# Optimization experiments

Hardware: AMD Instinct MI355X
Metric: run time of the kernel (lower is better)

## Reference

```python
import jax, jax.numpy as jnp
import numpy as np

L = 2          # num_bigbird_encoder_blocks
H = 8          # n_heads
BS = 64        # block_size
G = 2          # num_global_blocks
W = 3          # window_size (blocks)
EPS = 1e-8


def rmsnorm(x, w, eps=EPS):
    return x * jax.lax.rsqrt(jnp.mean(x * x, axis=-1, keepdims=True) + eps) * w


def setup_inputs() -> dict:
    key = jax.random.key(0)
    ks = jax.random.split(key, 12)
    B, S, D, F, V = 8, 2048, 256, 1024, 32000
    nB = S // BS
    inp = {
        "input_ids": jax.random.randint(ks[0], (B, S), 0, V, dtype=jnp.int64),
        "rand_idx": jax.random.randint(ks[1], (nB, 2), 0, nB, dtype=jnp.int32),
        "emb": jax.random.normal(ks[2], (V, D), jnp.float32) * 0.02,
        "ln1_w": jnp.ones((L, D), jnp.float32),
        "wq": jax.random.normal(ks[3], (L, D, D), jnp.float32) / np.sqrt(D),
        "wk": jax.random.normal(ks[4], (L, D, D), jnp.float32) / np.sqrt(D),
        "wv": jax.random.normal(ks[5], (L, D, D), jnp.float32) / np.sqrt(D),
        "wo": jax.random.normal(ks[6], (L, D, D), jnp.float32) / np.sqrt(D),
        "ln2_w": jnp.ones((L, D), jnp.float32),
        "w1": jax.random.normal(ks[7], (L, D, F), jnp.float32) / np.sqrt(D),
        "w2": jax.random.normal(ks[8], (L, F, D), jnp.float32) / np.sqrt(F),
        "final_ln_w": jnp.ones((D,), jnp.float32),
    }
    return inp


def _split_heads(x, B, nB, dh):
    # [B,S,D] -> [B,H,nB,bs,dh]
    return x.reshape(B, nB, BS, H, dh).transpose(0, 3, 1, 2, 4)


def reference(input_ids, rand_idx, emb, ln1_w, wq, wk, wv, wo, ln2_w, w1, w2, final_ln_w):
    B, S = input_ids.shape
    D = emb.shape[1]
    dh = D // H
    nB = S // BS
    scale = 1.0 / np.sqrt(dh)

    # block-sparse key-block indices per query block: global + sliding window + random
    blocks = jnp.arange(nB)
    win = jnp.clip(blocks[:, None] + jnp.arange(-(W // 2), W // 2 + 1)[None, :], 0, nB - 1)
    glob = jnp.broadcast_to(jnp.arange(G), (nB, G))
    idx = jnp.concatenate([glob, win, rand_idx.astype(jnp.int32)], axis=1)  # [nB, M], M=7
    M = idx.shape[1]

    x = emb[input_ids]  # [B,S,D]
    for l in range(L):
        h = rmsnorm(x, ln1_w[l])
        q = _split_heads(h @ wq[l], B, nB, dh)  # [B,H,nB,bs,dh]
        k = _split_heads(h @ wk[l], B, nB, dh)
        v = _split_heads(h @ wv[l], B, nB, dh)
        k_sel = k[:, :, idx]  # [B,H,nB,M,bs,dh]
        v_sel = v[:, :, idx]
        scores = jnp.einsum("bhnqd,bhnmsd->bhnqms", q, k_sel) * scale
        a = jax.nn.softmax(scores.reshape(B, H, nB, BS, M * BS), axis=-1)
        a = a.reshape(B, H, nB, BS, M, BS)
        o = jnp.einsum("bhnqms,bhnmsd->bhnqd", a, v_sel)
        o = o.transpose(0, 2, 3, 1, 4).reshape(B, S, D)
        x = x + o @ wo[l]
        h2 = rmsnorm(x, ln2_w[l])
        x = x + jax.nn.gelu(h2 @ w1[l]) @ w2[l]
    return rmsnorm(x, final_ln_w)
```

## Files before the change

kernel.cpp:

```cpp
#include <hip/hip_runtime.h>
#include <cstdint>
#include <cstddef>

typedef __bf16 bf16x8 __attribute__((ext_vector_type(8)));
typedef __bf16 bf16x4 __attribute__((ext_vector_type(4)));
typedef float  f32x4  __attribute__((ext_vector_type(4)));
typedef unsigned u32x2 __attribute__((ext_vector_type(2)));
typedef unsigned u32x4 __attribute__((ext_vector_type(4)));

#define DMODEL 256

__device__ __forceinline__ float bflo(unsigned u) { return __builtin_bit_cast(float, u << 16); }
__device__ __forceinline__ float bfhi(unsigned u) { return __builtin_bit_cast(float, u & 0xffff0000u); }
__device__ __forceinline__ unsigned short bfbits(float f) {
  return __builtin_bit_cast(unsigned short, (__bf16)f);
}

#define GLOAD_LDS16(gp, lp) __builtin_amdgcn_global_load_lds(                 \
    (const __attribute__((address_space(1))) unsigned*)(gp),                  \
    (__attribute__((address_space(3))) unsigned*)(lp), 16, 0, 0)

__global__ void transpose_all(const float* __restrict__ wq, const float* __restrict__ wk,
                              const float* __restrict__ wv, const float* __restrict__ wo,
                              const float* __restrict__ w1, const float* __restrict__ w2,
                              __bf16* __restrict__ wbase) {
  int idx = blockIdx.x * 256 + threadIdx.x;
  int l = idx >= 786432;
  int r = idx - l * 786432;
  __bf16* wb = wbase + (size_t)l * 786432;
  const float* s; __bf16* d; int R, C, e;
  if (r < 65536)       { s = wq + l * 65536;  d = wb;          R = 256;  C = 256;  e = r; }
  else if (r < 131072) { s = wk + l * 65536;  d = wb + 65536;  R = 256;  C = 256;  e = r - 65536; }
  else if (r < 196608) { s = wv + l * 65536;  d = wb + 131072; R = 256;  C = 256;  e = r - 131072; }
  else if (r < 262144) { s = wo + l * 65536;  d = wb + 196608; R = 256;  C = 256;  e = r - 196608; }
  else if (r < 524288) { s = w1 + l * 262144; d = wb + 262144; R = 256;  C = 1024; e = r - 262144; }
  else                 { s = w2 + l * 262144; d = wb + 524288; R = 1024; C = 256;  e = r - 524288; }
  int row = e / C, col = e - row * C;
  d[col * R + row] = (__bf16)s[e];
}

__global__ void embed_k(const int* __restrict__ ids, const float* __restrict__ emb, float* __restrict__ x) {
  int row = blockIdx.x * 4 + (threadIdx.x >> 6);
  int lane = threadIdx.x & 63;
  int id = ids[row];
  ((f32x4*)(x + (size_t)row * DMODEL))[lane] = ((const f32x4*)(emb + (size_t)id * DMODEL))[lane];
}

template<typename OUT>
__global__ void rmsnorm_k(const float* __restrict__ x, const float* __restrict__ w, OUT* __restrict__ out) {
  int row = blockIdx.x * 4 + (threadIdx.x >> 6);
  int lane = threadIdx.x & 63;
  f32x4 v = ((const f32x4*)(x + (size_t)row * DMODEL))[lane];
  float ss = v[0]*v[0] + v[1]*v[1] + v[2]*v[2] + v[3]*v[3];
  #pragma unroll
  for (int off = 1; off < 64; off <<= 1) ss += __shfl_xor(ss, off);
  float rms = rsqrtf(ss * (1.0f / DMODEL) + 1e-8f);
  f32x4 wv = ((const f32x4*)w)[lane];
  if constexpr (sizeof(OUT) == 4) {
    f32x4 o;
    o[0] = v[0]*rms*wv[0]; o[1] = v[1]*rms*wv[1]; o[2] = v[2]*rms*wv[2]; o[3] = v[3]*rms*wv[3];
    ((f32x4*)((float*)out + (size_t)row * DMODEL))[lane] = o;
  } else {
    bf16x4 o;
    o[0] = (__bf16)(v[0]*rms*wv[0]); o[1] = (__bf16)(v[1]*rms*wv[1]);
    o[2] = (__bf16)(v[2]*rms*wv[2]); o[3] = (__bf16)(v[3]*rms*wv[3]);
    ((bf16x4*)((__bf16*)out + (size_t)row * DMODEL))[lane] = o;
  }
}

__device__ __forceinline__ float gelu_f(float v) {
  return 0.5f * v * (1.0f + tanhf(0.7978845608028654f * (v + 0.044715f * v * v * v)));
}

template<bool RES, bool GELU, bool OUTB>
__launch_bounds__(256)
__global__ void gemm_bt(const __bf16* __restrict__ A, const __bf16* __restrict__ Bt,
                        __bf16* __restrict__ outb, float* __restrict__ res,
                        int K, int N) {
  __shared__ char sm[32768];
  int tid = threadIdx.x;
  int lane = tid & 63;
  int w = tid >> 6;
  int wr = w >> 1, wc = w & 1;
  int lr = lane & 15;
  int hk = lane >> 4;
  size_t bm = (size_t)blockIdx.x * 128, bn = (size_t)blockIdx.y * 128;
  const __bf16* Ab = A + bm * (size_t)K;
  const __bf16* Bb = Bt + bn * (size_t)K;

  int u0 = w * 128 + lane;
  int r0 = u0 >> 2, c0 = u0 & 3;
  int u1 = u0 + 64;
  int r1 = u1 >> 2, c1 = u1 & 3;
  size_t ga0 = (size_t)r0 * K + c0 * 8;
  size_t ga1 = (size_t)r1 * K + c1 * 8;
  int lb0 = (w * 2) * 1024;
  int lb1 = (w * 2 + 1) * 1024;

  int nt = K >> 5;
  GLOAD_LDS16(Ab + ga0, sm + lb0);
  GLOAD_LDS16(Bb + ga0, sm + 8192 + lb0);
  GLOAD_LDS16(Ab + ga1, sm + lb1);
  GLOAD_LDS16(Bb + ga1, sm + 8192 + lb1);
  __syncthreads();

  f32x4 acc[4][4] = {};
  for (int t = 0; t < nt; ++t) {
    char* cur = sm + (t & 1) * 16384;
    if (t + 1 < nt) {
      char* nxt = sm + ((t + 1) & 1) * 16384;
      int kk = (t + 1) * 32;
      GLOAD_LDS16(Ab + ga0 + kk, nxt + lb0);
      GLOAD_LDS16(Bb + ga0 + kk, nxt + 8192 + lb0);
      GLOAD_LDS16(Ab + ga1 + kk, nxt + lb1);
      GLOAD_LDS16(Bb + ga1 + kk, nxt + 8192 + lb1);
    }
    bf16x8 av[4], bv[4];
    #pragma unroll
    for (int i = 0; i < 4; ++i)
      av[i] = *(const bf16x8*)(cur + (wr * 64 + i * 16 + lr) * 64 + hk * 16);
    #pragma unroll
    for (int i = 0; i < 4; ++i)
      bv[i] = *(const bf16x8*)(cur + 8192 + (wc * 64 + i * 16 + lr) * 64 + hk * 16);
    #pragma unroll
    for (int mi = 0; mi < 4; ++mi)
      #pragma unroll
      for (int ni = 0; ni < 4; ++ni)
        acc[mi][ni] = __builtin_amdgcn_mfma_f32_16x16x32_bf16(av[mi], bv[ni], acc[mi][ni], 0, 0, 0);
    __syncthreads();
  }

  size_t row0 = bm + wr * 64 + (hk << 2);
  size_t col0 = bn + wc * 64 + lr;
  #pragma unroll
  for (int mi = 0; mi < 4; ++mi)
    #pragma unroll
    for (int ni = 0; ni < 4; ++ni)
      #pragma unroll
      for (int j = 0; j < 4; ++j) {
        size_t row = row0 + mi * 16 + j, col = col0 + ni * 16;
        float val = acc[mi][ni][j];
        if constexpr (GELU) val = gelu_f(val);
        if constexpr (RES)  res[row * N + col] += val;
        if constexpr (OUTB) outb[row * N + col] = (__bf16)val;
      }
}

#define ATTN_LDS 57344

__launch_bounds__(256)
__global__ void attn_k(const __bf16* __restrict__ qkv, const int* __restrict__ rand_idx,
                       __bf16* __restrict__ o) {
  extern __shared__ char sm[];
  char* smVt = sm + 28672;
  int tid = threadIdx.x;
  int lane = tid & 63;
  int w = tid >> 6;
  int q16 = lane & 15, g = lane >> 4;

  int bid0 = blockIdx.x;
  int bid = (bid0 & 7) * 256 + (bid0 >> 3);
  int b = bid >> 8;
  int hh = (bid >> 5) & 7;
  int n = bid & 31;
  int r5 = rand_idx[n * 2], r6 = rand_idx[n * 2 + 1];
  int nm1 = n > 0 ? n - 1 : 0;
  int np1 = n < 31 ? n + 1 : 31;
  size_t base = (size_t)b * 2048;

  #pragma unroll
  for (int it = 0; it < 7; ++it) {
    int chunk = it * 256 + tid;
    int r = chunk >> 2, c16 = chunk & 3;
    int m = r >> 6, si = r & 63;
    int kb = m == 0 ? 0 : m == 1 ? 1 : m == 2 ? nm1 : m == 3 ? n : m == 4 ? np1 : m == 5 ? r5 : r6;
    u32x4 d = *(const u32x4*)(qkv + (base + kb * 64 + si) * 768 + 256 + hh * 32 + c16 * 8);
    *(u32x4*)(sm + ((chunk * 16) ^ ((r & 7) << 4))) = d;
  }

  #pragma unroll
  for (int it = 0; it < 4; ++it) {
    int item = it * 256 + tid;
    if (item < 896) {
      int dp = item & 15, ko = item >> 4;
      int s0 = ko * 8;
      int m = s0 >> 6, si = s0 & 63;
      int kb = m == 0 ? 0 : m == 1 ? 1 : m == 2 ? nm1 : m == 3 ? n : m == 4 ? np1 : m == 5 ? r5 : r6;
      const unsigned* vs = (const unsigned*)(qkv + (base + kb * 64 + si) * 768 + 512 + hh * 32) + dp;
      unsigned vr[8];
      #pragma unroll
      for (int i = 0; i < 8; ++i) vr[i] = vs[(size_t)i * 384];
      u32x4 lo4, hi4;
      #pragma unroll
      for (int wd = 0; wd < 4; ++wd) {
        unsigned a = vr[2 * wd], bb = vr[2 * wd + 1];
        lo4[wd] = (a & 0xffffu) | (bb << 16);
        hi4[wd] = (a >> 16) | (bb & 0xffff0000u);
      }
      unsigned swz = (unsigned)((dp & 7) << 4);
      int byte0 = (2 * dp) * 896 + ko * 16;
      *(u32x4*)(smVt + (byte0 ^ swz)) = lo4;
      *(u32x4*)(smVt + ((byte0 + 896) ^ swz)) = hi4;
    }
  }

  bf16x8 qf = *(const bf16x8*)(qkv + (base + n * 64 + w * 16 + q16) * 768 + hh * 32 + g * 8);

  __syncthreads();

  const float SC  = 0.17677669529663687f * 1.4426950408889634f;
  const float THR = 8.0f / SC;
  int src0 = q16 + 32 * (g & 1);
  int src1 = src0 + 16;
  bool hi = (g >= 2);
  float m_run = -1e30f, mc = 0.f, ssum = 0.f;
  f32x4 oacc[2] = {};
  bool first = true;

  #pragma unroll
  for (int c = 0; c < 7; ++c) {
    f32x4 st[4];
    #pragma unroll
    for (int tl = 0; tl < 4; ++tl) {
      int row = 16 * (4 * c + tl) + q16;
      bf16x8 kf = *(const bf16x8*)(sm + ((row * 64 + g * 16) ^ ((q16 & 7) << 4)));
      st[tl] = __builtin_amdgcn_mfma_f32_16x16x32_bf16(kf, qf, (f32x4){0.f, 0.f, 0.f, 0.f}, 0, 0, 0);
    }
    float lm = st[0][0];
    #pragma unroll
    for (int tl = 0; tl < 4; ++tl) {
      lm = fmaxf(lm, fmaxf(fmaxf(st[tl][0], st[tl][1]), fmaxf(st[tl][2], st[tl][3])));
    }
    lm = fmaxf(lm, __shfl_xor(lm, 16));
    lm = fmaxf(lm, __shfl_xor(lm, 32));
    if (first || !__all(lm <= m_run + THR)) {
      float nm = fmaxf(m_run, lm);
      float sf = __builtin_amdgcn_exp2f((m_run - nm) * SC);
      ssum *= sf;
      #pragma unroll
      for (int dt = 0; dt < 2; ++dt)
        #pragma unroll
        for (int j = 0; j < 4; ++j) oacc[dt][j] *= sf;
      m_run = nm;
      mc = nm * SC;
      first = false;
    }
    unsigned pk0[4], pk1[4];
    #pragma unroll
    for (int tl = 0; tl < 4; ++tl) {
      float e0 = __builtin_amdgcn_exp2f(fmaf(st[tl][0], SC, -mc));
      float e1 = __builtin_amdgcn_exp2f(fmaf(st[tl][1], SC, -mc));
      float e2 = __builtin_amdgcn_exp2f(fmaf(st[tl][2], SC, -mc));
      float e3 = __builtin_amdgcn_exp2f(fmaf(st[tl][3], SC, -mc));
      ssum += (e0 + e1) + (e2 + e3);
      pk0[tl] = (unsigned)bfbits(e0) | ((unsigned)bfbits(e1) << 16);
      pk1[tl] = (unsigned)bfbits(e2) | ((unsigned)bfbits(e3) << 16);
    }
    #pragma unroll
    for (int ksl = 0; ksl < 2; ++ksl) {
      int ks = 2 * c + ksl;
      int lt0 = 2 * ksl, lt1 = 2 * ksl + 1;
      unsigned a0 = __shfl(pk0[lt0], src0), b0 = __shfl(pk0[lt1], src0);
      unsigned a1 = __shfl(pk1[lt0], src0), b1 = __shfl(pk1[lt1], src0);
      unsigned a2 = __shfl(pk0[lt0], src1), b2 = __shfl(pk0[lt1], src1);
      unsigned a3 = __shfl(pk1[lt0], src1), b3 = __shfl(pk1[lt1], src1);
      u32x4 pw;
      pw[0] = hi ? b0 : a0; pw[1] = hi ? b1 : a1;
      pw[2] = hi ? b2 : a2; pw[3] = hi ? b3 : a3;
      bf16x8 pf = __builtin_bit_cast(bf16x8, pw);
      #pragma unroll
      for (int dt = 0; dt < 2; ++dt) {
        int d = 16 * dt + q16;
        bf16x8 vf = *(const bf16x8*)(smVt + ((d * 896 + 64 * ks + 16 * g) ^ (((d >> 1) & 7) << 4)));
        oacc[dt] = __builtin_amdgcn_mfma_f32_16x16x32_bf16(vf, pf, oacc[dt], 0, 0, 0);
      }
    }
  }

  ssum += __shfl_xor(ssum, 16);
  ssum += __shfl_xor(ssum, 32);
  float inv = 1.0f / ssum;
  size_t orow = (base + n * 64 + w * 16 + q16) * 256 + hh * 32;
  #pragma unroll
  for (int dt = 0; dt < 2; ++dt) {
    u32x2 pk;
    pk[0] = (unsigned)bfbits(oacc[dt][0] * inv) | ((unsigned)bfbits(oacc[dt][1] * inv) << 16);
    pk[1] = (unsigned)bfbits(oacc[dt][2] * inv) | ((unsigned)bfbits(oacc[dt][3] * inv) << 16);
    *(u32x2*)(o + orow + 16 * dt + 4 * g) = pk;
  }
}

extern "C" void kernel_launch(void* const* d_in, const int* in_sizes, int n_in,
                              void* d_out, int out_size, void* d_ws, size_t ws_size,
                              hipStream_t stream) {
  const int*   ids      = (const int*)d_in[0];
  const int*   rand_idx = (const int*)d_in[1];
  const float* emb      = (const float*)d_in[2];
  const float* ln1      = (const float*)d_in[3];
  const float* wq       = (const float*)d_in[4];
  const float* wk       = (const float*)d_in[5];
  const float* wv       = (const float*)d_in[6];
  const float* wo       = (const float*)d_in[7];
  const float* ln2      = (const float*)d_in[8];
  const float* w1       = (const float*)d_in[9];
  const float* w2       = (const float*)d_in[10];
  const float* fln      = (const float*)d_in[11];
  float* out = (float*)d_out;

  char* ws = (char*)d_ws;
  float*  x    = (float*)ws;
  __bf16* h    = (__bf16*)(ws + 16777216);
  __bf16* qkv  = (__bf16*)(ws + 25165824);
  __bf16* obuf = (__bf16*)(ws + 50331648);
  __bf16* g    = qkv;
  __bf16* wbase = (__bf16*)(ws + 58720256);

  transpose_all<<<6144, 256, 0, stream>>>(wq, wk, wv, wo, w1, w2, wbase);
  embed_k<<<4096, 256, 0, stream>>>(ids, emb, x);

  for (int l = 0; l < 2; ++l) {
    __bf16* qkvT = wbase + (size_t)l * 786432;
    __bf16* woT  = qkvT + 196608;
    __bf16* w1T  = woT + 65536;
    __bf16* w2T  = w1T + 262144;

    rmsnorm_k<__bf16><<<4096, 256, 0, stream>>>(x, ln1 + (size_t)l * 256, h);
    gemm_bt<false, false, true><<<dim3(128, 6), 256, 0, stream>>>(h, qkvT, qkv, nullptr, 256, 768);
    attn_k<<<2048, 256, ATTN_LDS, stream>>>(qkv, rand_idx, obuf);
    gemm_bt<true, false, false><<<dim3(128, 2), 256, 0, stream>>>(obuf, woT, nullptr, x, 256, 256);
    rmsnorm_k<__bf16><<<4096, 256, 0, stream>>>(x, ln2 + (size_t)l * 256, h);
    gemm_bt<false, true, true><<<dim3(128, 8), 256, 0, stream>>>(h, w1T, g, nullptr, 256, 1024);
    gemm_bt<true, false, false><<<dim3(128, 2), 256, 0, stream>>>(g, w2T, nullptr, x, 1024, 256);
  }

  rmsnorm_k<float><<<4096, 256, 0, stream>>>(x, fln, out);
}
```

Measured before the change: 400.2 us.

## Pipeline attention key/value blocks through double-buffered LDS, add BM=64 GEMM tiles

The attention kernel no longer stages all seven key/value blocks into a large LDS buffer before computing. It now streams one block at a time through a small double buffer, with register prefetch of the next block overlapping the current block's MFMA work. This cuts LDS use from 56KB to 16KB so more workgroups fit per CU. The GEMM gains a BM template parameter, and the N=256 GEMMs (output projection and w2) use 64-row tiles so they launch twice as many workgroups. GELU's tanh is replaced by an exp2/rcp sigmoid form, which is mathematically equivalent but at slightly different precision.

Result: faster. 335.6 us (-16.2%).

```diff
diff --git a/kernel.cpp b/kernel.cpp
--- a/kernel.cpp
+++ b/kernel.cpp
@@ -10,8 +10,6 @@
 
 #define DMODEL 256
 
-__device__ __forceinline__ float bflo(unsigned u) { return __builtin_bit_cast(float, u << 16); }
-__device__ __forceinline__ float bfhi(unsigned u) { return __builtin_bit_cast(float, u & 0xffff0000u); }
 __device__ __forceinline__ unsigned short bfbits(float f) {
   return __builtin_bit_cast(unsigned short, (__bf16)f);
 }
@@ -69,71 +67,82 @@
 }
 
 __device__ __forceinline__ float gelu_f(float v) {
-  return 0.5f * v * (1.0f + tanhf(0.7978845608028654f * (v + 0.044715f * v * v * v)));
-}
-
-template<bool RES, bool GELU, bool OUTB>
+  float u = v + 0.044715f * v * v * v;
+  float s = __builtin_amdgcn_exp2f(-2.3022080898f * u);
+  return v * __builtin_amdgcn_rcpf(1.0f + s);
+}
+
+template<int BM, bool RES, bool GELU, bool OUTB>
 __launch_bounds__(256)
 __global__ void gemm_bt(const __bf16* __restrict__ A, const __bf16* __restrict__ Bt,
                         __bf16* __restrict__ outb, float* __restrict__ res,
                         int K, int N) {
-  __shared__ char sm[32768];
+  constexpr int WTM = BM / 2;
+  constexpr int MT = WTM / 16;
+  constexpr int ABYTES = BM * 64;
+  constexpr int TILE = ABYTES + 8192;
+  constexpr int LOADS = BM / 64 + 2;
+  __shared__ char sm[2 * TILE];
   int tid = threadIdx.x;
   int lane = tid & 63;
   int w = tid >> 6;
   int wr = w >> 1, wc = w & 1;
   int lr = lane & 15;
   int hk = lane >> 4;
-  size_t bm = (size_t)blockIdx.x * 128, bn = (size_t)blockIdx.y * 128;
+  size_t bm = (size_t)blockIdx.x * BM, bn = (size_t)blockIdx.y * 128;
   const __bf16* Ab = A + bm * (size_t)K;
   const __bf16* Bb = Bt + bn * (size_t)K;
 
-  int u0 = w * 128 + lane;
-  int r0 = u0 >> 2, c0 = u0 & 3;
-  int u1 = u0 + 64;
-  int r1 = u1 >> 2, c1 = u1 & 3;
-  size_t ga0 = (size_t)r0 * K + c0 * 8;
-  size_t ga1 = (size_t)r1 * K + c1 * 8;
-  int lb0 = (w * 2) * 1024;
-  int lb1 = (w * 2 + 1) * 1024;
+  const __bf16* gsrc[LOADS];
+  int ldst[LOADS];
+  #pragma unroll
+  for (int i = 0; i < LOADS; ++i) {
+    int chunk = i * 256 + tid;
+    if (chunk < BM * 4) {
+      int r = chunk >> 2, c16 = chunk & 3;
+      gsrc[i] = Ab + (size_t)r * K + c16 * 8;
+      ldst[i] = chunk * 16;
+    } else {
+      int cb = chunk - BM * 4;
+      int r = cb >> 2, c16 = cb & 3;
+      gsrc[i] = Bb + (size_t)r * K + c16 * 8;
+      ldst[i] = ABYTES + cb * 16;
+    }
+  }
 
   int nt = K >> 5;
-  GLOAD_LDS16(Ab + ga0, sm + lb0);
-  GLOAD_LDS16(Bb + ga0, sm + 8192 + lb0);
-  GLOAD_LDS16(Ab + ga1, sm + lb1);
-  GLOAD_LDS16(Bb + ga1, sm + 8192 + lb1);
+  #pragma unroll
+  for (int i = 0; i < LOADS; ++i) GLOAD_LDS16(gsrc[i], sm + ldst[i]);
   __syncthreads();
 
-  f32x4 acc[4][4] = {};
+  f32x4 acc[MT][4] = {};
   for (int t = 0; t < nt; ++t) {
-    char* cur = sm + (t & 1) * 16384;
+    char* cur = sm + (t & 1) * TILE;
     if (t + 1 < nt) {
-      char* nxt = sm + ((t + 1) & 1) * 16384;
+      char* nxt = sm + ((t + 1) & 1) * TILE;
       int kk = (t + 1) * 32;
-      GLOAD_LDS16(Ab + ga0 + kk, nxt + lb0);
-      GLOAD_LDS16(Bb + ga0 + kk, nxt + 8192 + lb0);
-      GLOAD_LDS16(Ab + ga1 + kk, nxt + lb1);
-      GLOAD_LDS16(Bb + ga1 + kk, nxt + 8192 + lb1);
-    }
-    bf16x8 av[4], bv[4];
+      #pragma unroll
+      for (int i = 0; i < LOADS; ++i) GLOAD_LDS16(gsrc[i] + kk, nxt + ldst[i]);
+    }
+    bf16x8 av[MT], bv[4];
+    #pragma unroll
+    for (int i = 0; i < MT; ++i)
+      av[i] = *(const bf16x8*)(cur + (wr * WTM + i * 16 + lr) * 64 + hk * 16);
     #pragma unroll
     for (int i = 0; i < 4; ++i)
-      av[i] = *(const bf16x8*)(cur + (wr * 64 + i * 16 + lr) * 64 + hk * 16);
-    #pragma unroll
-    for (int i = 0; i < 4; ++i)
-      bv[i] = *(const bf16x8*)(cur + 8192 + (wc * 64 + i * 16 + lr) * 64 + hk * 16);
-    #pragma unroll
-    for (int mi = 0; mi < 4; ++mi)
+      bv[i] = *(const bf16x8*)(cur + ABYTES + (wc * 64 + i * 16 + lr) * 64 + hk * 16);
+    #pragma unroll
+    for (int mi = 0; mi < MT; ++mi)
       #pragma unroll
       for (int ni = 0; ni < 4; ++ni)
         acc[mi][ni] = __builtin_amdgcn_mfma_f32_16x16x32_bf16(av[mi], bv[ni], acc[mi][ni], 0, 0, 0);
     __syncthreads();
   }
 
-  size_t row0 = bm + wr * 64 + (hk << 2);
+  size_t row0 = bm + wr * WTM + (hk << 2);
   size_t col0 = bn + wc * 64 + lr;
   #pragma unroll
-  for (int mi = 0; mi < 4; ++mi)
+  for (int mi = 0; mi < MT; ++mi)
     #pragma unroll
     for (int ni = 0; ni < 4; ++ni)
       #pragma unroll
@@ -146,13 +155,13 @@
       }
 }
 
-#define ATTN_LDS 57344
+#define ATTN_LDS 16384
+#define ABUF 8192
 
 __launch_bounds__(256)
 __global__ void attn_k(const __bf16* __restrict__ qkv, const int* __restrict__ rand_idx,
                        __bf16* __restrict__ o) {
   extern __shared__ char sm[];
-  char* smVt = sm + 28672;
   int tid = threadIdx.x;
   int lane = tid & 63;
   int w = tid >> 6;
@@ -167,46 +176,12 @@
   int nm1 = n > 0 ? n - 1 : 0;
   int np1 = n < 31 ? n + 1 : 31;
   size_t base = (size_t)b * 2048;
-
-  #pragma unroll
-  for (int it = 0; it < 7; ++it) {
-    int chunk = it * 256 + tid;
-    int r = chunk >> 2, c16 = chunk & 3;
-    int m = r >> 6, si = r & 63;
-    int kb = m == 0 ? 0 : m == 1 ? 1 : m == 2 ? nm1 : m == 3 ? n : m == 4 ? np1 : m == 5 ? r5 : r6;
-    u32x4 d = *(const u32x4*)(qkv + (base + kb * 64 + si) * 768 + 256 + hh * 32 + c16 * 8);
-    *(u32x4*)(sm + ((chunk * 16) ^ ((r & 7) << 4))) = d;
-  }
-
-  #pragma unroll
-  for (int it = 0; it < 4; ++it) {
-    int item = it * 256 + tid;
-    if (item < 896) {
-      int dp = item & 15, ko = item >> 4;
-      int s0 = ko * 8;
-      int m = s0 >> 6, si = s0 & 63;
-      int kb = m == 0 ? 0 : m == 1 ? 1 : m == 2 ? nm1 : m == 3 ? n : m == 4 ? np1 : m == 5 ? r5 : r6;
-      const unsigned* vs = (const unsigned*)(qkv + (base + kb * 64 + si) * 768 + 512 + hh * 32) + dp;
-      unsigned vr[8];
-      #pragma unroll
-      for (int i = 0; i < 8; ++i) vr[i] = vs[(size_t)i * 384];
-      u32x4 lo4, hi4;
-      #pragma unroll
-      for (int wd = 0; wd < 4; ++wd) {
-        unsigned a = vr[2 * wd], bb = vr[2 * wd + 1];
-        lo4[wd] = (a & 0xffffu) | (bb << 16);
-        hi4[wd] = (a >> 16) | (bb & 0xffff0000u);
-      }
-      unsigned swz = (unsigned)((dp & 7) << 4);
-      int byte0 = (2 * dp) * 896 + ko * 16;
-      *(u32x4*)(smVt + (byte0 ^ swz)) = lo4;
-      *(u32x4*)(smVt + ((byte0 + 896) ^ swz)) = hi4;
-    }
-  }
+  int kbs[7] = {0, 1, nm1, n, np1, r5, r6};
+
+  int ksi = tid >> 2, kc16 = tid & 3;
+  int vdp = tid & 15, vko = tid >> 4;
 
   bf16x8 qf = *(const bf16x8*)(qkv + (base + n * 64 + w * 16 + q16) * 768 + hh * 32 + g * 8);
-
-  __syncthreads();
 
   const float SC  = 0.17677669529663687f * 1.4426950408889634f;
   const float THR = 8.0f / SC;
@@ -217,20 +192,48 @@
   f32x4 oacc[2] = {};
   bool first = true;
 
+  u32x4 kreg;
+  unsigned vr0, vr1, vr2, vr3;
+  {
+    int kb = kbs[0];
+    kreg = *(const u32x4*)(qkv + (base + kb * 64 + ksi) * 768 + 256 + hh * 32 + kc16 * 8);
+    const unsigned* vs = (const unsigned*)(qkv + (base + kb * 64 + vko * 4) * 768 + 512 + hh * 32) + vdp;
+    vr0 = vs[0]; vr1 = vs[384]; vr2 = vs[768]; vr3 = vs[1152];
+  }
+  {
+    char* bp = sm;
+    *(u32x4*)(bp + ((tid * 16) ^ (((tid >> 2) & 7) << 4))) = kreg;
+    u32x2 lo2, hi2;
+    lo2[0] = (vr0 & 0xffffu) | (vr1 << 16);  lo2[1] = (vr2 & 0xffffu) | (vr3 << 16);
+    hi2[0] = (vr0 >> 16) | (vr1 & 0xffff0000u); hi2[1] = (vr2 >> 16) | (vr3 & 0xffff0000u);
+    unsigned swz = (unsigned)((vdp & 7) << 4);
+    int byte0 = vdp * 256 + vko * 8;
+    *(u32x2*)(bp + 4096 + (byte0 ^ swz)) = lo2;
+    *(u32x2*)(bp + 4096 + ((byte0 + 128) ^ swz)) = hi2;
+  }
+  __syncthreads();
+
   #pragma unroll
   for (int c = 0; c < 7; ++c) {
+    char* cur = sm + (c & 1) * ABUF;
+    if (c < 6) {
+      int kb = kbs[c + 1];
+      kreg = *(const u32x4*)(qkv + (base + kb * 64 + ksi) * 768 + 256 + hh * 32 + kc16 * 8);
+      const unsigned* vs = (const unsigned*)(qkv + (base + kb * 64 + vko * 4) * 768 + 512 + hh * 32) + vdp;
+      vr0 = vs[0]; vr1 = vs[384]; vr2 = vs[768]; vr3 = vs[1152];
+    }
+
     f32x4 st[4];
     #pragma unroll
     for (int tl = 0; tl < 4; ++tl) {
-      int row = 16 * (4 * c + tl) + q16;
-      bf16x8 kf = *(const bf16x8*)(sm + ((row * 64 + g * 16) ^ ((q16 & 7) << 4)));
+      int row = 16 * tl + q16;
+      bf16x8 kf = *(const bf16x8*)(cur + ((row * 64 + g * 16) ^ ((q16 & 7) << 4)));
       st[tl] = __builtin_amdgcn_mfma_f32_16x16x32_bf16(kf, qf, (f32x4){0.f, 0.f, 0.f, 0.f}, 0, 0, 0);
     }
     float lm = st[0][0];
     #pragma unroll
-    for (int tl = 0; tl < 4; ++tl) {
+    for (int tl = 0; tl < 4; ++tl)
       lm = fmaxf(lm, fmaxf(fmaxf(st[tl][0], st[tl][1]), fmaxf(st[tl][2], st[tl][3])));
-    }
     lm = fmaxf(lm, __shfl_xor(lm, 16));
     lm = fmaxf(lm, __shfl_xor(lm, 32));
     if (first || !__all(lm <= m_run + THR)) {
@@ -258,7 +261,6 @@
     }
     #pragma unroll
     for (int ksl = 0; ksl < 2; ++ksl) {
-      int ks = 2 * c + ksl;
       int lt0 = 2 * ksl, lt1 = 2 * ksl + 1;
       unsigned a0 = __shfl(pk0[lt0], src0), b0 = __shfl(pk0[lt1], src0);
       unsigned a1 = __shfl(pk1[lt0], src0), b1 = __shfl(pk1[lt1], src0);
@@ -271,9 +273,22 @@
       #pragma unroll
       for (int dt = 0; dt < 2; ++dt) {
         int d = 16 * dt + q16;
-        bf16x8 vf = *(const bf16x8*)(smVt + ((d * 896 + 64 * ks + 16 * g) ^ (((d >> 1) & 7) << 4)));
+        bf16x8 vf = *(const bf16x8*)(cur + 4096 + ((d * 128 + 64 * ksl + 16 * g) ^ (((d >> 1) & 7) << 4)));
         oacc[dt] = __builtin_amdgcn_mfma_f32_16x16x32_bf16(vf, pf, oacc[dt], 0, 0, 0);
       }
+    }
+
+    if (c < 6) {
+      char* nxt = sm + ((c + 1) & 1) * ABUF;
+      *(u32x4*)(nxt + ((tid * 16) ^ (((tid >> 2) & 7) << 4))) = kreg;
+      u32x2 lo2, hi2;
+      lo2[0] = (vr0 & 0xffffu) | (vr1 << 16);  lo2[1] = (vr2 & 0xffffu) | (vr3 << 16);
+      hi2[0] = (vr0 >> 16) | (vr1 & 0xffff0000u); hi2[1] = (vr2 >> 16) | (vr3 & 0xffff0000u);
+      unsigned swz = (unsigned)((vdp & 7) << 4);
+      int byte0 = vdp * 256 + vko * 8;
+      *(u32x2*)(nxt + 4096 + (byte0 ^ swz)) = lo2;
+      *(u32x2*)(nxt + 4096 + ((byte0 + 128) ^ swz)) = hi2;
+      __syncthreads();
     }
   }
 
@@ -325,12 +340,12 @@
     __bf16* w2T  = w1T + 262144;
 
     rmsnorm_k<__bf16><<<4096, 256, 0, stream>>>(x, ln1 + (size_t)l * 256, h);
-    gemm_bt<false, false, true><<<dim3(128, 6), 256, 0, stream>>>(h, qkvT, qkv, nullptr, 256, 768);
+    gemm_bt<128, false, false, true><<<dim3(128, 6), 256, 0, stream>>>(h, qkvT, qkv, nullptr, 256, 768);
     attn_k<<<2048, 256, ATTN_LDS, stream>>>(qkv, rand_idx, obuf);
-    gemm_bt<true, false, false><<<dim3(128, 2), 256, 0, stream>>>(obuf, woT, nullptr, x, 256, 256);
+    gemm_bt<64, true, false, false><<<dim3(256, 2), 256, 0, stream>>>(obuf, woT, nullptr, x, 256, 256);
     rmsnorm_k<__bf16><<<4096, 256, 0, stream>>>(x, ln2 + (size_t)l * 256, h);
-    gemm_bt<false, true, true><<<dim3(128, 8), 256, 0, stream>>>(h, w1T, g, nullptr, 256, 1024);
-    gemm_bt<true, false, false><<<dim3(128, 2), 256, 0, stream>>>(g, w2T, nullptr, x, 1024, 256);
+    gemm_bt<128, false, true, true><<<dim3(128, 8), 256, 0, stream>>>(h, w1T, g, nullptr, 256, 1024);
+    gemm_bt<64, true, false, false><<<dim3(256, 2), 256, 0, stream>>>(g, w2T, nullptr, x, 1024, 256);
   }
 
   rmsnorm_k<float><<<4096, 256, 0, stream>>>(x, fln, out);
```
